# Performance work log

Hardware: AMD Instinct MI355X
Metric: run time of the kernel (lower is better)

The kernel has to match this reference:

```python
import jax, jax.numpy as jnp
import numpy as np

B, C, H, W = 16, 256, 96, 96
P = 16          # num_prototypes
G = 8           # GroupNorm groups
EPS = 1e-5


def setup_inputs() -> dict:
    key = jax.random.key(0)
    ks = jax.random.split(key, 18)
    n = jax.random.normal
    return {
        "x": n(ks[0], (B, C, H, W), jnp.float32),
        "prototypes": n(ks[1], (1, P, C), jnp.float32),
        "pos_embed": n(ks[2], (1, C, 64, 64), jnp.float32) * 0.02,
        "q_w": n(ks[3], (C, C), jnp.float32) * (C ** -0.5),
        "q_b": n(ks[4], (C,), jnp.float32) * 0.01,
        "k_w": n(ks[5], (C, C), jnp.float32) * (C ** -0.5),
        "k_b": n(ks[6], (C,), jnp.float32) * 0.01,
        "v_w": n(ks[7], (C, C), jnp.float32) * (C ** -0.5),
        "v_b": n(ks[8], (C,), jnp.float32) * 0.01,
        "out_w": n(ks[9], (C, C), jnp.float32) * (C ** -0.5),
        "out_b": n(ks[10], (C,), jnp.float32) * 0.01,
        "dw_w": n(ks[11], (C, 1, 3, 3), jnp.float32) * (1.0 / 3.0),  # depthwise 3x3, no bias
        "bn_g": 1.0 + 0.1 * n(ks[12], (C,), jnp.float32),
        "bn_b": 0.1 * n(ks[13], (C,), jnp.float32),
        "bn_mean": 0.05 * n(ks[14], (C,), jnp.float32),
        "bn_var": 0.5 + jax.random.uniform(ks[15], (C,), jnp.float32),
        "gn_g": 1.0 + 0.1 * n(ks[16], (C,), jnp.float32),
        "gn_b": 0.1 * n(ks[17], (C,), jnp.float32),
    }


def _forward(x, prototypes, pos_embed, q_w, q_b, k_w, k_b, v_w, v_b,
             out_w, out_b, dw_w, bn_g, bn_b, bn_mean, bn_var, gn_g, gn_b):
    b, c, h, w = x.shape
    residual = x

    # bilinear interpolation of learnable PE (half-pixel centers == align_corners=False)
    pos = jax.image.resize(pos_embed, (1, c, h, w), method="bilinear")
    xp = x + pos

    # 1x1 conv Q projection -> [B, HW, C]
    q = jnp.einsum("bchw,dc->bhwd", xp, q_w) + q_b          # [B,H,W,C]
    q = q.reshape(b, h * w, c)

    # K/V from tiny prototype set (shared across batch) -> [P, C]
    k = prototypes[0] @ k_w.T + k_b
    v = prototypes[0] @ v_w.T + v_b

    # attention over only P=16 keys
    scale = c ** (-0.5)
    attn = jax.nn.softmax(jnp.einsum("bnc,pc->bnp", q, k) * scale, axis=-1)
    out = jnp.einsum("bnp,pc->bnc", attn, v)                # [B,HW,C]
    out = out.reshape(b, h, w, c).transpose(0, 3, 1, 2)     # [B,C,H,W]

    # 1x1 conv out projection
    out = jnp.einsum("bchw,dc->bdhw", out, out_w) + out_b[None, :, None, None]

    # local branch: depthwise 3x3 conv -> BN (eval, running stats) -> GELU(exact)
    dw = jax.lax.conv_general_dilated(
        out, dw_w, window_strides=(1, 1), padding="SAME",
        feature_group_count=c, dimension_numbers=("NCHW", "OIHW", "NCHW"))
    inv = (bn_g / jnp.sqrt(bn_var + EPS))[None, :, None, None]
    bn = (dw - bn_mean[None, :, None, None]) * inv + bn_b[None, :, None, None]
    out = out + jax.nn.gelu(bn, approximate=False)

    # GroupNorm(8, C) over residual sum
    y = out + residual
    yg = y.reshape(b, G, c // G, h, w)
    mu = yg.mean(axis=(2, 3, 4), keepdims=True)
    var = yg.var(axis=(2, 3, 4), keepdims=True)
    yn = ((yg - mu) * jax.lax.rsqrt(var + EPS)).reshape(b, c, h, w)
    return yn * gn_g[None, :, None, None] + gn_b[None, :, None, None]


def reference(x, prototypes, pos_embed, q_w, q_b, k_w, k_b, v_w, v_b,
              out_w, out_b, dw_w, bn_g, bn_b, bn_mean, bn_var, gn_g, gn_b):
    return _forward(x, prototypes, pos_embed, q_w, q_b, k_w, k_b, v_w, v_b,
                    out_w, out_b, dw_w, bn_g, bn_b, bn_mean, bn_var, gn_g, gn_b)
```

## Files before the change

kernel.cpp:

```cpp
#include <hip/hip_runtime.h>
#include <math.h>

#define C_   256
#define B_   16
#define HW_  9216
#define W_   96
#define H_   96
#define P_   16
#define EPS_ 1e-5f

typedef unsigned int u32;

__global__ __launch_bounds__(256) void k_kv(
    const float* __restrict__ proto, const float* __restrict__ kw,
    const float* __restrict__ kb, const float* __restrict__ vw,
    const float* __restrict__ vb, float* __restrict__ wk, float* __restrict__ wv,
    float* __restrict__ sums)
{
    __shared__ float pr[C_];
    const int p = blockIdx.x, d = threadIdx.x;
    if (p == 0) sums[d] = 0.f;
    pr[d] = proto[p * C_ + d];
    __syncthreads();
    float kk = kb[d], vv = vb[d];
    const float* kr = kw + d * C_;
    const float* vr = vw + d * C_;
    #pragma unroll 8
    for (int c = 0; c < C_; ++c) {
        const float pc = pr[c];
        kk = fmaf(pc, kr[c], kk);
        vv = fmaf(pc, vr[c], vv);
    }
    wk[p * C_ + d] = kk;
    wv[p * C_ + d] = vv;
}

__global__ __launch_bounds__(256) void k_mu(
    const float* __restrict__ wk, const float* __restrict__ wv,
    const float* __restrict__ qw, const float* __restrict__ qb,
    const float* __restrict__ ow,
    float* __restrict__ wm, float* __restrict__ wu, float* __restrict__ ws0)
{
    __shared__ float row[C_];
    __shared__ float red[C_];
    const int blk = blockIdx.x, t = threadIdx.x;
    if (blk < 16) {
        const int p = blk;
        row[t] = wk[p * C_ + t];
        __syncthreads();
        float mm = 0.f;
        #pragma unroll 8
        for (int d = 0; d < C_; ++d)
            mm = fmaf(row[d], qw[d * C_ + t], mm);
        wm[t * P_ + p] = mm;
        red[t] = qb[t] * row[t];
        __syncthreads();
        for (int s = 128; s > 0; s >>= 1) {
            if (t < s) red[t] += red[t + s];
            __syncthreads();
        }
        if (t == 0) ws0[p] = red[0];
    } else {
        const int p = blk - 16;
        row[t] = wv[p * C_ + t];
        __syncthreads();
        float uu = 0.f;
        const float* orow = ow + t * C_;
        #pragma unroll 8
        for (int c = 0; c < C_; ++c)
            uu = fmaf(row[c], orow[c], uu);
        wu[t * P_ + p] = uu;
    }
}

__global__ __launch_bounds__(256) void k_pd(
    const float* __restrict__ pos, const float* __restrict__ m,
    float* __restrict__ pd)
{
    const int n = blockIdx.x * 256 + threadIdx.x;
    const int h = n / W_, w = n - h * W_;
    float sy = (h + 0.5f) * (2.0f / 3.0f) - 0.5f;
    float sx = (w + 0.5f) * (2.0f / 3.0f) - 0.5f;
    sy = fminf(fmaxf(sy, 0.f), 63.f);
    sx = fminf(fmaxf(sx, 0.f), 63.f);
    const int y0 = (int)sy, x0 = (int)sx;
    const float fy = sy - (float)y0, fx = sx - (float)x0;
    const int y1 = min(y0 + 1, 63), x1 = min(x0 + 1, 63);
    const float w00 = (1.f - fy) * (1.f - fx), w01 = (1.f - fy) * fx;
    const float w10 = fy * (1.f - fx),         w11 = fy * fx;
    const int i00 = y0 * 64 + x0, i01 = y0 * 64 + x1;
    const int i10 = y1 * 64 + x0, i11 = y1 * 64 + x1;

    float acc[P_];
    #pragma unroll
    for (int p = 0; p < P_; ++p) acc[p] = 0.f;

    #pragma unroll 4
    for (int c = 0; c < C_; ++c) {
        const float* pc = pos + c * 4096;
        const float pv = pc[i00] * w00 + pc[i01] * w01 +
                         pc[i10] * w10 + pc[i11] * w11;
        #pragma unroll
        for (int p = 0; p < P_; ++p)
            acc[p] = fmaf(pv, m[c * P_ + p], acc[p]);
    }
    #pragma unroll
    for (int p = 0; p < P_; ++p) pd[p * HW_ + n] = acc[p];
}

__global__ __launch_bounds__(256) void k_attn(
    const float* __restrict__ x, const float* __restrict__ m,
    const float* __restrict__ u, const float* __restrict__ s0,
    const float* __restrict__ pd, const float* __restrict__ outb,
    float* __restrict__ o2)
{
    const int b = blockIdx.y;
    const int n0 = (blockIdx.x * 256 + threadIdx.x) * 2;
    const float* xp = x + (size_t)b * (C_ * HW_) + n0;

    float acc0[P_], acc1[P_];
    #pragma unroll
    for (int p = 0; p < P_; ++p) { acc0[p] = 0.f; acc1[p] = 0.f; }

    for (int cc = 0; cc < C_; cc += 8) {
        float2 xv[8];
        #pragma unroll
        for (int j = 0; j < 8; ++j)
            xv[j] = *reinterpret_cast<const float2*>(xp + (size_t)(cc + j) * HW_);
        #pragma unroll
        for (int j = 0; j < 8; ++j) {
            const float* mr = m + (cc + j) * P_;
            #pragma unroll
            for (int p = 0; p < P_; ++p) {
                acc0[p] = fmaf(xv[j].x, mr[p], acc0[p]);
                acc1[p] = fmaf(xv[j].y, mr[p], acc1[p]);
            }
        }
    }

    float l0[P_], l1[P_];
    float mx0 = -1e30f, mx1 = -1e30f;
    #pragma unroll
    for (int p = 0; p < P_; ++p) {
        const float2 pv = *reinterpret_cast<const float2*>(pd + (size_t)p * HW_ + n0);
        l0[p] = (acc0[p] + pv.x + s0[p]) * 0.0625f;
        l1[p] = (acc1[p] + pv.y + s0[p]) * 0.0625f;
        mx0 = fmaxf(mx0, l0[p]);
        mx1 = fmaxf(mx1, l1[p]);
    }
    float sum0 = 0.f, sum1 = 0.f;
    #pragma unroll
    for (int p = 0; p < P_; ++p) {
        l0[p] = __expf(l0[p] - mx0); sum0 += l0[p];
        l1[p] = __expf(l1[p] - mx1); sum1 += l1[p];
    }
    const float r0 = 1.f / sum0, r1 = 1.f / sum1;
    #pragma unroll
    for (int p = 0; p < P_; ++p) { l0[p] *= r0; l1[p] *= r1; }

    float* op = o2 + (size_t)b * (C_ * HW_) + n0;
    #pragma unroll 4
    for (int d = 0; d < C_; ++d) {
        const float* ur = u + d * P_;
        float o0 = outb[d], o1 = o0;
        #pragma unroll
        for (int p = 0; p < P_; ++p) {
            o0 = fmaf(l0[p], ur[p], o0);
            o1 = fmaf(l1[p], ur[p], o1);
        }
        *reinterpret_cast<float2*>(op + (size_t)d * HW_) = make_float2(o0, o1);
    }
}

__global__ __launch_bounds__(256) void k_local(
    const float* __restrict__ x,
    const float* __restrict__ dww, const float* __restrict__ bng,
    const float* __restrict__ bnb, const float* __restrict__ bnm,
    const float* __restrict__ bnv,
    float* __restrict__ y, float* __restrict__ sums)
{
    __shared__ float tile[98 * 100];
    const int c = blockIdx.x, b = blockIdx.y, t = threadIdx.x;

    if (t < 100) { tile[t] = 0.f; tile[97 * 100 + t] = 0.f; }
    if (t < 96)  { tile[(t + 1) * 100 + 1] = 0.f; tile[(t + 1) * 100 + 98] = 0.f; }

    const size_t plane = (size_t)(b * C_ + c) * HW_;
    const float4* op4 = reinterpret_cast<const float4*>(y + plane);
    #pragma unroll
    for (int k = 0; k < 9; ++k) {
        const int g = t + k * 256;
        const int h = g / 24;
        const int w0 = (g - h * 24) * 4;
        const float4 v = op4[g];
        const int base = (h + 1) * 100 + w0 + 2;
        *reinterpret_cast<float2*>(&tile[base])     = make_float2(v.x, v.y);
        *reinterpret_cast<float2*>(&tile[base + 2]) = make_float2(v.z, v.w);
    }
    __syncthreads();

    const float w00 = dww[c * 9 + 0], w01 = dww[c * 9 + 1], w02 = dww[c * 9 + 2];
    const float w10 = dww[c * 9 + 3], w11 = dww[c * 9 + 4], w12 = dww[c * 9 + 5];
    const float w20 = dww[c * 9 + 6], w21 = dww[c * 9 + 7], w22 = dww[c * 9 + 8];
    const float inv  = bng[c] * rsqrtf(bnv[c] + EPS_);
    const float mu   = bnm[c];
    const float beta = bnb[c];

    const float4* xp4 = reinterpret_cast<const float4*>(x + plane);
    float4* yp4 = reinterpret_cast<float4*>(y + plane);
    float s1 = 0.f, s2 = 0.f;

    #pragma unroll
    for (int k = 0; k < 9; ++k) {
        const int g = t + k * 256;
        const float4 xv = xp4[g];
        const int h = g / 24;
        const int w0 = (g - h * 24) * 4;
        const int r0 = h * 100 + w0;
        const float4 a0 = *reinterpret_cast<const float4*>(&tile[r0]);
        const float4 a1 = *reinterpret_cast<const float4*>(&tile[r0 + 4]);
        const float4 b0 = *reinterpret_cast<const float4*>(&tile[r0 + 100]);
        const float4 b1 = *reinterpret_cast<const float4*>(&tile[r0 + 104]);
        const float4 c0 = *reinterpret_cast<const float4*>(&tile[r0 + 200]);
        const float4 c1 = *reinterpret_cast<const float4*>(&tile[r0 + 204]);
        const float A[8]  = {a0.x, a0.y, a0.z, a0.w, a1.x, a1.y, a1.z, a1.w};
        const float Bv[8] = {b0.x, b0.y, b0.z, b0.w, b1.x, b1.y, b1.z, b1.w};
        const float Cv[8] = {c0.x, c0.y, c0.z, c0.w, c1.x, c1.y, c1.z, c1.w};
        const float xs[4] = {xv.x, xv.y, xv.z, xv.w};
        float ys[4];
        #pragma unroll
        for (int j = 0; j < 4; ++j) {
            float dwv = A[j + 1] * w00 + A[j + 2] * w01 + A[j + 3] * w02
                      + Bv[j + 1] * w10 + Bv[j + 2] * w11 + Bv[j + 3] * w12
                      + Cv[j + 1] * w20 + Cv[j + 2] * w21 + Cv[j + 3] * w22;
            const float bn = (dwv - mu) * inv + beta;
            const float gl = 0.5f * bn * (1.f + erff(bn * 0.70710678118654752f));
            const float yv = Bv[j + 2] + gl + xs[j];
            s1 += yv;
            s2 = fmaf(yv, yv, s2);
            ys[j] = yv;
        }
        yp4[g] = make_float4(ys[0], ys[1], ys[2], ys[3]);
    }

    __syncthreads();
    float* red = tile;
    red[t] = s1; red[256 + t] = s2;
    __syncthreads();
    for (int s = 128; s > 0; s >>= 1) {
        if (t < s) { red[t] += red[t + s]; red[256 + t] += red[256 + t + s]; }
        __syncthreads();
    }
    if (t == 0) {
        const int bg = b * 8 + (c >> 5);
        atomicAdd(&sums[bg * 2 + 0], red[0]);
        atomicAdd(&sums[bg * 2 + 1], red[256]);
    }
}

__global__ __launch_bounds__(256) void k_norm(
    const float* __restrict__ sums, const float* __restrict__ gng,
    const float* __restrict__ gnb, float* __restrict__ y)
{
    const u32 i0 = ((u32)blockIdx.x * 256u + threadIdx.x) * 4u;
    const u32 plane = i0 / HW_;
    const u32 c = plane & 255u;
    const u32 b = plane >> 8;
    const u32 bg = b * 8u + (c >> 5);
    const float cntinv = 1.f / 294912.f;
    const float mean = sums[bg * 2 + 0] * cntinv;
    const float var  = fmaf(sums[bg * 2 + 1], cntinv, -mean * mean);
    const float inv  = rsqrtf(var + EPS_);
    const float a  = gng[c] * inv;
    const float bb = gnb[c] - mean * a;

    float4 v = *reinterpret_cast<const float4*>(y + i0);
    v.x = fmaf(v.x, a, bb);
    v.y = fmaf(v.y, a, bb);
    v.z = fmaf(v.z, a, bb);
    v.w = fmaf(v.w, a, bb);
    *reinterpret_cast<float4*>(y + i0) = v;
}

extern "C" void kernel_launch(void* const* d_in, const int* in_sizes, int n_in,
                              void* d_out, int out_size, void* d_ws, size_t ws_size,
                              hipStream_t stream)
{
    const float* x     = (const float*)d_in[0];
    const float* proto = (const float*)d_in[1];
    const float* pos   = (const float*)d_in[2];
    const float* qw    = (const float*)d_in[3];
    const float* qb    = (const float*)d_in[4];
    const float* kw    = (const float*)d_in[5];
    const float* kb    = (const float*)d_in[6];
    const float* vw    = (const float*)d_in[7];
    const float* vb    = (const float*)d_in[8];
    const float* ow    = (const float*)d_in[9];
    const float* ob    = (const float*)d_in[10];
    const float* dww   = (const float*)d_in[11];
    const float* bng   = (const float*)d_in[12];
    const float* bnb   = (const float*)d_in[13];
    const float* bnm   = (const float*)d_in[14];
    const float* bnv   = (const float*)d_in[15];
    const float* gng   = (const float*)d_in[16];
    const float* gnb   = (const float*)d_in[17];

    char* ws = (char*)d_ws;
    float* sums = (float*)(ws);
    float* s0   = (float*)(ws + 1024);
    float* wk   = (float*)(ws + 2048);
    float* wv   = (float*)(ws + 2048 + 16384);
    float* wm   = (float*)(ws + 2048 + 2 * 16384);
    float* wu   = (float*)(ws + 2048 + 3 * 16384);
    float* pd   = (float*)(ws + 2048 + 4 * 16384);

    float* out = (float*)d_out;

    k_kv<<<16, 256, 0, stream>>>(proto, kw, kb, vw, vb, wk, wv, sums);
    k_mu<<<32, 256, 0, stream>>>(wk, wv, qw, qb, ow, wm, wu, s0);
    k_pd<<<36, 256, 0, stream>>>(pos, wm, pd);
    k_attn<<<dim3(18, 16), 256, 0, stream>>>(x, wm, wu, s0, pd, ob, out);
    k_local<<<dim3(256, 16), 256, 0, stream>>>(x, dww, bng, bnb, bnm, bnv, out, sums);
    k_norm<<<36864, 256, 0, stream>>>(sums, gng, gnb, out);
}
```

Measured before the change: 533.4 us.

## Split fused attention kernel into logits/softmax and output-projection kernels

The single attention kernel, which ran only 288 blocks of 256 threads, is split into two kernels. The first computes logits and softmax per pixel with 2304 small blocks and writes the attention weights to a workspace buffer. The second reads those weights and computes the output projection with a 3D grid of 4608 blocks, each writing 8 output channels. The aim is more parallelism and occupancy. The cost is an extra round trip to global memory for the 16xHW weights per batch and one more launch.

Result: no change. 528.6 us (-0.9%).

```diff
diff --git a/kernel.cpp b/kernel.cpp
--- a/kernel.cpp
+++ b/kernel.cpp
@@ -108,67 +108,80 @@
     for (int p = 0; p < P_; ++p) pd[p * HW_ + n] = acc[p];
 }
 
-__global__ __launch_bounds__(256) void k_attn(
+__global__ __launch_bounds__(64) void k_logits(
     const float* __restrict__ x, const float* __restrict__ m,
-    const float* __restrict__ u, const float* __restrict__ s0,
-    const float* __restrict__ pd, const float* __restrict__ outb,
-    float* __restrict__ o2)
-{
-    const int b = blockIdx.y;
-    const int n0 = (blockIdx.x * 256 + threadIdx.x) * 2;
-    const float* xp = x + (size_t)b * (C_ * HW_) + n0;
-
-    float acc0[P_], acc1[P_];
-    #pragma unroll
-    for (int p = 0; p < P_; ++p) { acc0[p] = 0.f; acc1[p] = 0.f; }
-
-    for (int cc = 0; cc < C_; cc += 8) {
-        float2 xv[8];
-        #pragma unroll
-        for (int j = 0; j < 8; ++j)
-            xv[j] = *reinterpret_cast<const float2*>(xp + (size_t)(cc + j) * HW_);
-        #pragma unroll
-        for (int j = 0; j < 8; ++j) {
+    const float* __restrict__ s0, const float* __restrict__ pd,
+    float* __restrict__ lw)
+{
+    const int n = blockIdx.x * 64 + threadIdx.x;
+    const int b = n / HW_;
+    const int npx = n - b * HW_;
+    const float* xp = x + (size_t)b * (C_ * HW_) + npx;
+
+    float acc[P_];
+    #pragma unroll
+    for (int p = 0; p < P_; ++p) acc[p] = 0.f;
+
+    for (int cc = 0; cc < C_; cc += 16) {
+        float xv[16];
+        #pragma unroll
+        for (int j = 0; j < 16; ++j)
+            xv[j] = xp[(size_t)(cc + j) * HW_];
+        #pragma unroll
+        for (int j = 0; j < 16; ++j) {
             const float* mr = m + (cc + j) * P_;
             #pragma unroll
-            for (int p = 0; p < P_; ++p) {
-                acc0[p] = fmaf(xv[j].x, mr[p], acc0[p]);
-                acc1[p] = fmaf(xv[j].y, mr[p], acc1[p]);
-            }
+            for (int p = 0; p < P_; ++p)
+                acc[p] = fmaf(xv[j], mr[p], acc[p]);
         }
     }
 
-    float l0[P_], l1[P_];
-    float mx0 = -1e30f, mx1 = -1e30f;
+    float l[P_];
+    float mx = -1e30f;
     #pragma unroll
     for (int p = 0; p < P_; ++p) {
-        const float2 pv = *reinterpret_cast<const float2*>(pd + (size_t)p * HW_ + n0);
-        l0[p] = (acc0[p] + pv.x + s0[p]) * 0.0625f;
-        l1[p] = (acc1[p] + pv.y + s0[p]) * 0.0625f;
-        mx0 = fmaxf(mx0, l0[p]);
-        mx1 = fmaxf(mx1, l1[p]);
-    }
-    float sum0 = 0.f, sum1 = 0.f;
-    #pragma unroll
-    for (int p = 0; p < P_; ++p) {
-        l0[p] = __expf(l0[p] - mx0); sum0 += l0[p];
-        l1[p] = __expf(l1[p] - mx1); sum1 += l1[p];
-    }
-    const float r0 = 1.f / sum0, r1 = 1.f / sum1;
-    #pragma unroll
-    for (int p = 0; p < P_; ++p) { l0[p] *= r0; l1[p] *= r1; }
-
-    float* op = o2 + (size_t)b * (C_ * HW_) + n0;
-    #pragma unroll 4
-    for (int d = 0; d < C_; ++d) {
+        l[p] = (acc[p] + pd[(size_t)p * HW_ + npx] + s0[p]) * 0.0625f;
+        mx = fmaxf(mx, l[p]);
+    }
+    float sum = 0.f;
+    #pragma unroll
+    for (int p = 0; p < P_; ++p) { l[p] = __expf(l[p] - mx); sum += l[p]; }
+    const float r = 1.f / sum;
+
+    float* lp = lw + (size_t)b * (P_ * HW_) + npx;
+    #pragma unroll
+    for (int p = 0; p < P_; ++p) lp[(size_t)p * HW_] = l[p] * r;
+}
+
+__global__ __launch_bounds__(256) void k_out(
+    const float* __restrict__ lw, const float* __restrict__ u,
+    const float* __restrict__ ob, float* __restrict__ o2)
+{
+    const int b = blockIdx.z;
+    const int d0 = blockIdx.y * 8;
+    const int px = blockIdx.x * 1024 + threadIdx.x * 4;
+
+    const float* lp = lw + (size_t)b * (P_ * HW_) + px;
+    float4 lv[P_];
+    #pragma unroll
+    for (int p = 0; p < P_; ++p)
+        lv[p] = *reinterpret_cast<const float4*>(lp + (size_t)p * HW_);
+
+    float* op = o2 + ((size_t)b * C_ + d0) * HW_ + px;
+    #pragma unroll
+    for (int j = 0; j < 8; ++j) {
+        const int d = d0 + j;
         const float* ur = u + d * P_;
-        float o0 = outb[d], o1 = o0;
+        const float obd = ob[d];
+        float4 o = make_float4(obd, obd, obd, obd);
         #pragma unroll
         for (int p = 0; p < P_; ++p) {
-            o0 = fmaf(l0[p], ur[p], o0);
-            o1 = fmaf(l1[p], ur[p], o1);
+            o.x = fmaf(lv[p].x, ur[p], o.x);
+            o.y = fmaf(lv[p].y, ur[p], o.y);
+            o.z = fmaf(lv[p].z, ur[p], o.z);
+            o.w = fmaf(lv[p].w, ur[p], o.w);
         }
-        *reinterpret_cast<float2*>(op + (size_t)d * HW_) = make_float2(o0, o1);
+        *reinterpret_cast<float4*>(op + (size_t)j * HW_) = o;
     }
 }
 
@@ -313,13 +326,15 @@
     float* wm   = (float*)(ws + 2048 + 2 * 16384);
     float* wu   = (float*)(ws + 2048 + 3 * 16384);
     float* pd   = (float*)(ws + 2048 + 4 * 16384);
+    float* lw   = (float*)(ws + 2048 + 4 * 16384 + 589824);
 
     float* out = (float*)d_out;
 
     k_kv<<<16, 256, 0, stream>>>(proto, kw, kb, vw, vb, wk, wv, sums);
     k_mu<<<32, 256, 0, stream>>>(wk, wv, qw, qb, ow, wm, wu, s0);
     k_pd<<<36, 256, 0, stream>>>(pos, wm, pd);
-    k_attn<<<dim3(18, 16), 256, 0, stream>>>(x, wm, wu, s0, pd, ob, out);
+    k_logits<<<2304, 64, 0, stream>>>(x, wm, s0, pd, lw);
+    k_out<<<dim3(9, 32, 16), 256, 0, stream>>>(lw, wu, ob, out);
     k_local<<<dim3(256, 16), 256, 0, stream>>>(x, dww, bng, bnb, bnm, bnv, out, sums);
     k_norm<<<36864, 256, 0, stream>>>(sums, gng, gnb, out);
 }
```
